# Kernel optimization log

Measured on AMD Instinct MI355X. Metric: run time of the kernel, lower is better.

The kernel has to match this reference:

```python
import jax, jax.numpy as jnp
import numpy as np

# TTCReward hyperparameters (init_kwargs)
LONG_TH = 0.0
LAT_TH = 0.0
H = 4               # num_historical_intervals
LEAST_MIN_TTC = 0.95
DT = 0.5            # time_span_per_interval

NUM_EGO = 32        # scenes (len(ptr) - 1)
AGENTS_PER = 128
N_AGENTS = NUM_EGO * AGENTS_PER   # 4096
T_TOTAL = 34


def setup_inputs():
    key = jax.random.key(0)
    k1, k2, k3, k4 = jax.random.split(key, 4)
    infer_position = jax.random.uniform(k1, (N_AGENTS, T_TOTAL, 2), jnp.float32) * 100.0
    infer_heading = (jax.random.uniform(k2, (N_AGENTS, T_TOTAL), jnp.float32) - 0.5) * (2.0 * np.pi)
    box = jax.random.uniform(k3, (N_AGENTS, 4), jnp.float32) * 1.5 + 0.5  # front/rear/left/right extents
    infer_valid_mask = jax.random.uniform(k4, (N_AGENTS, T_TOTAL)) > 0.05
    batch = jnp.repeat(jnp.arange(NUM_EGO, dtype=jnp.int32), AGENTS_PER)
    ptr = jnp.arange(NUM_EGO + 1, dtype=jnp.int32) * AGENTS_PER
    return dict(infer_position=infer_position, infer_heading=infer_heading, box=box,
                infer_valid_mask=infer_valid_mask, batch=batch, ptr=ptr)


def _corners(pos, yaw, box):
    # pos [N,T,2], yaw [N,T], box [N,4] = (front, rear, left, right) extents
    f, r, l, rt = box[:, 0], box[:, 1], box[:, 2], box[:, 3]
    local = jnp.stack([jnp.stack([f, l], -1), jnp.stack([f, -rt], -1),
                       jnp.stack([-r, -rt], -1), jnp.stack([-r, l], -1)], axis=1)  # [N,4,2]
    c = jnp.cos(yaw)[:, :, None]
    s = jnp.sin(yaw)[:, :, None]
    lx = local[:, None, :, 0]
    ly = local[:, None, :, 1]
    x = lx * c - ly * s + pos[:, :, None, 0]
    y = lx * s + ly * c + pos[:, :, None, 1]
    return jnp.stack([x, y], -1)  # [N,T,4,2]


def _loss(lx, ly, bf, br, bl, brt):
    # min over 4 box-side clamped penetrations, then max over the 4 corners (last axis)
    long_t = jnp.minimum(jnp.maximum(bf + LONG_TH - lx, 0.0),
                         jnp.maximum(br + LONG_TH + lx, 0.0))
    lat_t = jnp.minimum(jnp.maximum(bl + LAT_TH - ly, 0.0),
                        jnp.maximum(brt + LAT_TH + ly, 0.0))
    return jnp.max(jnp.minimum(long_t, lat_t), axis=-1)


def reference(infer_position, infer_heading, box, infer_valid_mask, batch, ptr):
    N = infer_heading.shape[0]
    vel = (infer_position[:, H:] - infer_position[:, H - 1:-1]) / DT
    pos = infer_position[:, H:] + vel * LEAST_MIN_TTC           # [N,T,2] position at min-TTC horizon
    yaw = infer_heading[:, H:]                                  # [N,T]
    corner = _corners(pos, yaw, box)                            # [N,T,4,2]

    ego = ptr[:-1]                                              # [B]
    B = ego.shape[0]
    Tn = pos.shape[1]

    ego_pos = jnp.swapaxes(pos[ego], 0, 1)                      # [T,B,2]
    ego_yaw = jnp.swapaxes(yaw[ego], 0, 1)                      # [T,B]
    ego_corner = jnp.swapaxes(corner[ego], 0, 1)                # [T,B,4,2]
    ego_box = box[ego]                                          # [B,4]
    agent_pos = jnp.swapaxes(pos, 0, 1)                         # [T,N,2]
    agent_yaw = jnp.swapaxes(yaw, 0, 1)                         # [T,N]
    agent_corner = jnp.swapaxes(corner, 0, 1)                   # [T,N,4,2]

    valid = infer_valid_mask[:, H:]                             # [N,T]
    edge_mask = (valid[ego].T[:, :, None] & valid.T[:, None, :]
                 & (batch[ego][:, None] == batch[None, :])[None]
                 & (ego[:, None] != jnp.arange(N)[None, :])[None])  # [T,B,N]

    # ego corners expressed in each agent's local frame, vs agent box
    d = ego_corner[:, :, None] - agent_pos[:, None, :, None]   # [T,B,N,4,2]
    ca = jnp.cos(agent_yaw)[:, None, :, None]
    sa = jnp.sin(agent_yaw)[:, None, :, None]
    ego_in_agent = _loss(d[..., 0] * ca + d[..., 1] * sa,
                         -d[..., 0] * sa + d[..., 1] * ca,
                         box[:, 0][None, None, :, None], box[:, 1][None, None, :, None],
                         box[:, 2][None, None, :, None], box[:, 3][None, None, :, None])  # [T,B,N]

    # agent corners expressed in each ego's local frame, vs ego box
    d2 = agent_corner[:, None] - ego_pos[:, :, None, None]     # [T,B,N,4,2]
    ce = jnp.cos(ego_yaw)[:, :, None, None]
    se = jnp.sin(ego_yaw)[:, :, None, None]
    agent_in_ego = _loss(d2[..., 0] * ce + d2[..., 1] * se,
                         -d2[..., 0] * se + d2[..., 1] * ce,
                         ego_box[:, 0][None, :, None, None], ego_box[:, 1][None, :, None, None],
                         ego_box[:, 2][None, :, None, None], ego_box[:, 3][None, :, None, None])  # [T,B,N]

    # Replicate original dense_to_sparse edge orderings: ego_in_agent edges enumerate
    # edge_mask in (t,i,j) order; agent_in_ego edges use the transposed (t,j,i) order.
    # The torch code max-combines the two lists per *position* e before scatter_max
    # over rows t*B+i (taken from the (t,i,j) ordering), which we reproduce exactly
    # via rank-based scatters into fixed-size [E] buffers.
    E = Tn * B * N
    rows = jnp.broadcast_to((jnp.arange(Tn)[:, None] * B + jnp.arange(B)[None, :])[:, :, None],
                            (Tn, B, N)).reshape(-1)
    m = edge_mask.reshape(-1)
    idx = jnp.where(m, jnp.cumsum(m.astype(jnp.int32)) - 1, E)      # OOB index E -> dropped
    mT = jnp.swapaxes(edge_mask, 1, 2).reshape(-1)
    idxT = jnp.where(mT, jnp.cumsum(mT.astype(jnp.int32)) - 1, E)
    neg_inf = jnp.float32(-jnp.inf)
    b_by_rank = jnp.full((E,), neg_inf).at[idx].set(ego_in_agent.reshape(-1))
    a_by_rank = jnp.full((E,), neg_inf).at[idxT].set(jnp.swapaxes(agent_in_ego, 1, 2).reshape(-1))
    rows_by_rank = jnp.zeros((E,), jnp.int32).at[idx].set(rows.astype(jnp.int32))
    ttc_loss = jnp.maximum(a_by_rank, b_by_rank)
    seg_max = jax.ops.segment_max(ttc_loss, rows_by_rank, num_segments=Tn * B)  # empty -> -inf
    # reward per ego: all timesteps have max ttc_loss <= 0 (no edge -> -inf -> True)
    return jnp.all((seg_max <= 0.0).reshape(Tn, B), axis=0).astype(jnp.float32)
```

## Files before the change

kernel.cpp:

```cpp
#include <hip/hip_runtime.h>
#include <math.h>

#define NUM_EGO    32
#define AGENTS_PER 128
#define T_TOTAL    34
#define H_OFF      4
#define TN         30
#define SCALE      1.9f

__global__ __launch_bounds__(AGENTS_PER) void ttc_main(
    const float* __restrict__ posg,
    const float* __restrict__ headg,
    const float* __restrict__ boxg,
    const int*   __restrict__ validg,
    const int*   __restrict__ ptrg,
    float* __restrict__ out)
{
    const int blk = blockIdx.x;
    const int b   = blk / TN;
    const int t   = blk % TN;
    const int tt  = t + H_OFF;
    const int a   = threadIdx.x;

    const int e0 = ptrg[b];
    const int n  = e0 + a;

    const int   ev   = validg[e0 * T_TOTAL + tt];
    const float2 ep1 = *(const float2*)&posg[(e0 * T_TOTAL + tt) * 2];
    const float2 ep0 = *(const float2*)&posg[(e0 * T_TOTAL + tt - 1) * 2];
    const float eyaw = headg[e0 * T_TOTAL + tt];
    const float4 ebx = *(const float4*)&boxg[e0 * 4];
    const int   av   = validg[n * T_TOTAL + tt];
    const float2 ap1 = *(const float2*)&posg[(n * T_TOTAL + tt) * 2];
    const float2 ap0 = *(const float2*)&posg[(n * T_TOTAL + tt - 1) * 2];
    const float ayaw = headg[n * T_TOTAL + tt];
    const float4 abx = *(const float4*)&boxg[n * 4];

    const float ex = ep1.x + SCALE * (ep1.x - ep0.x);
    const float ey = ep1.y + SCALE * (ep1.y - ep0.y);
    const float ax = ap1.x + SCALE * (ap1.x - ap0.x);
    const float ay = ap1.y + SCALE * (ap1.y - ap0.y);
    const float ce = __cosf(eyaw), se = __sinf(eyaw);
    const float ca = __cosf(ayaw), sa = __sinf(ayaw);

    const float ef = ebx.x, er = ebx.y, el = ebx.z, ert = ebx.w;
    const float af = abx.x, ar = abx.y, al = abx.z, art = abx.w;

    const float elx[4] = { ef,  ef, -er, -er };
    const float ely[4] = { el, -ert, -ert,  el };
    const float alx[4] = { af,  af, -ar, -ar };
    const float aly[4] = { al, -art, -art,  al };

    float L1 = 0.0f;
    #pragma unroll
    for (int k = 0; k < 4; ++k) {
        float cxw = elx[k] * ce - ely[k] * se + ex;
        float cyw = elx[k] * se + ely[k] * ce + ey;
        float dx = cxw - ax;
        float dy = cyw - ay;
        float lx =  dx * ca + dy * sa;
        float ly = -dx * sa + dy * ca;
        float lo = fminf(fmaxf(af - lx, 0.0f), fmaxf(ar + lx, 0.0f));
        float la = fminf(fmaxf(al - ly, 0.0f), fmaxf(art + ly, 0.0f));
        L1 = fmaxf(L1, fminf(lo, la));
    }

    float L2 = 0.0f;
    #pragma unroll
    for (int k = 0; k < 4; ++k) {
        float cxw = alx[k] * ca - aly[k] * sa + ax;
        float cyw = alx[k] * sa + aly[k] * ca + ay;
        float dx = cxw - ex;
        float dy = cyw - ey;
        float lx =  dx * ce + dy * se;
        float ly = -dx * se + dy * ce;
        float lo = fminf(fmaxf(ef - lx, 0.0f), fmaxf(er + lx, 0.0f));
        float la = fminf(fmaxf(el - ly, 0.0f), fmaxf(ert + ly, 0.0f));
        L2 = fmaxf(L2, fminf(lo, la));
    }

    const bool hit = (a != 0) & (ev != 0) & (av != 0) &
                     (fmaxf(L1, L2) > 0.0f);

    if (__any(hit) && (threadIdx.x & 63) == 0) {
        out[b] = 0.0f;
    }
}

extern "C" void kernel_launch(void* const* d_in, const int* in_sizes, int n_in,
                              void* d_out, int out_size, void* d_ws, size_t ws_size,
                              hipStream_t stream) {
    const float* posg   = (const float*)d_in[0];
    const float* headg  = (const float*)d_in[1];
    const float* boxg   = (const float*)d_in[2];
    const int*   validg = (const int*)  d_in[3];
    const int*   ptrg   = (const int*)  d_in[5];
    float* out = (float*)d_out;

    hipMemsetD32Async((hipDeviceptr_t)out, 0x3F800000, NUM_EGO, stream);
    ttc_main<<<NUM_EGO * TN, AGENTS_PER, 0, stream>>>(
        posg, headg, boxg, validg, ptrg, out);
}
```

Measured before the change: 67.51 us.

## Fuse timesteps into one block per ego and drop separate memset

Launches one 768-thread block per ego scene, with six groups of threads each walking five consecutive timesteps. Previous positions are carried forward between steps, and sincos is computed in one call. A shared-memory OR reduction now writes the final 0/1 output directly, so the memset launch is no longer needed. This removes one launch and the cross-block writes, but only 32 blocks run, which leaves most of the GPU idle and lengthens each thread's serial work.

```diff
diff --git a/kernel.cpp b/kernel.cpp
--- a/kernel.cpp
+++ b/kernel.cpp
@@ -8,7 +8,11 @@
 #define TN         30
 #define SCALE      1.9f
 
-__global__ __launch_bounds__(AGENTS_PER) void ttc_main(
+#define BLOCK  768
+#define TPG    5
+#define NWAVES (BLOCK / 64)
+
+__global__ __launch_bounds__(BLOCK) void ttc_fused(
     const float* __restrict__ posg,
     const float* __restrict__ headg,
     const float* __restrict__ boxg,
@@ -16,33 +20,15 @@
     const int*   __restrict__ ptrg,
     float* __restrict__ out)
 {
-    const int blk = blockIdx.x;
-    const int b   = blk / TN;
-    const int t   = blk % TN;
-    const int tt  = t + H_OFF;
-    const int a   = threadIdx.x;
+    const int b   = blockIdx.x;
+    const int tid = threadIdx.x;
+    const int a   = tid & (AGENTS_PER - 1);
+    const int g   = tid >> 7;
+    const int e0  = ptrg[b];
+    const int n   = e0 + a;
 
-    const int e0 = ptrg[b];
-    const int n  = e0 + a;
-
-    const int   ev   = validg[e0 * T_TOTAL + tt];
-    const float2 ep1 = *(const float2*)&posg[(e0 * T_TOTAL + tt) * 2];
-    const float2 ep0 = *(const float2*)&posg[(e0 * T_TOTAL + tt - 1) * 2];
-    const float eyaw = headg[e0 * T_TOTAL + tt];
     const float4 ebx = *(const float4*)&boxg[e0 * 4];
-    const int   av   = validg[n * T_TOTAL + tt];
-    const float2 ap1 = *(const float2*)&posg[(n * T_TOTAL + tt) * 2];
-    const float2 ap0 = *(const float2*)&posg[(n * T_TOTAL + tt - 1) * 2];
-    const float ayaw = headg[n * T_TOTAL + tt];
     const float4 abx = *(const float4*)&boxg[n * 4];
-
-    const float ex = ep1.x + SCALE * (ep1.x - ep0.x);
-    const float ey = ep1.y + SCALE * (ep1.y - ep0.y);
-    const float ax = ap1.x + SCALE * (ap1.x - ap0.x);
-    const float ay = ap1.y + SCALE * (ap1.y - ap0.y);
-    const float ce = __cosf(eyaw), se = __sinf(eyaw);
-    const float ca = __cosf(ayaw), sa = __sinf(ayaw);
-
     const float ef = ebx.x, er = ebx.y, el = ebx.z, ert = ebx.w;
     const float af = abx.x, ar = abx.y, al = abx.z, art = abx.w;
 
@@ -51,39 +37,76 @@
     const float alx[4] = { af,  af, -ar, -ar };
     const float aly[4] = { al, -art, -art,  al };
 
-    float L1 = 0.0f;
+    bool anyhit = false;
+
+    const int t0  = g * TPG;
+    const int tt0 = t0 + H_OFF;
+    float2 eprev = *(const float2*)&posg[(e0 * T_TOTAL + tt0 - 1) * 2];
+    float2 aprev = *(const float2*)&posg[(n  * T_TOTAL + tt0 - 1) * 2];
+
     #pragma unroll
-    for (int k = 0; k < 4; ++k) {
-        float cxw = elx[k] * ce - ely[k] * se + ex;
-        float cyw = elx[k] * se + ely[k] * ce + ey;
-        float dx = cxw - ax;
-        float dy = cyw - ay;
-        float lx =  dx * ca + dy * sa;
-        float ly = -dx * sa + dy * ca;
-        float lo = fminf(fmaxf(af - lx, 0.0f), fmaxf(ar + lx, 0.0f));
-        float la = fminf(fmaxf(al - ly, 0.0f), fmaxf(art + ly, 0.0f));
-        L1 = fmaxf(L1, fminf(lo, la));
+    for (int i = 0; i < TPG; ++i) {
+        const int tt = tt0 + i;
+
+        const int    ev   = validg[e0 * T_TOTAL + tt];
+        const int    av   = validg[n  * T_TOTAL + tt];
+        const float2 ecur = *(const float2*)&posg[(e0 * T_TOTAL + tt) * 2];
+        const float2 acur = *(const float2*)&posg[(n  * T_TOTAL + tt) * 2];
+        const float  eyaw = headg[e0 * T_TOTAL + tt];
+        const float  ayaw = headg[n  * T_TOTAL + tt];
+
+        const float ex = ecur.x + SCALE * (ecur.x - eprev.x);
+        const float ey = ecur.y + SCALE * (ecur.y - eprev.y);
+        const float ax = acur.x + SCALE * (acur.x - aprev.x);
+        const float ay = acur.y + SCALE * (acur.y - aprev.y);
+        eprev = ecur; aprev = acur;
+
+        float se, ce, sa, ca;
+        __sincosf(eyaw, &se, &ce);
+        __sincosf(ayaw, &sa, &ca);
+
+        float L1 = 0.0f;
+        #pragma unroll
+        for (int k = 0; k < 4; ++k) {
+            float cxw = elx[k] * ce - ely[k] * se + ex;
+            float cyw = elx[k] * se + ely[k] * ce + ey;
+            float dx = cxw - ax;
+            float dy = cyw - ay;
+            float lx =  dx * ca + dy * sa;
+            float ly = -dx * sa + dy * ca;
+            float lo = fminf(fmaxf(af - lx, 0.0f), fmaxf(ar + lx, 0.0f));
+            float la = fminf(fmaxf(al - ly, 0.0f), fmaxf(art + ly, 0.0f));
+            L1 = fmaxf(L1, fminf(lo, la));
+        }
+
+        float L2 = 0.0f;
+        #pragma unroll
+        for (int k = 0; k < 4; ++k) {
+            float cxw = alx[k] * ca - aly[k] * sa + ax;
+            float cyw = alx[k] * sa + aly[k] * ca + ay;
+            float dx = cxw - ex;
+            float dy = cyw - ey;
+            float lx =  dx * ce + dy * se;
+            float ly = -dx * se + dy * ce;
+            float lo = fminf(fmaxf(ef - lx, 0.0f), fmaxf(er + lx, 0.0f));
+            float la = fminf(fmaxf(el - ly, 0.0f), fmaxf(ert + ly, 0.0f));
+            L2 = fmaxf(L2, fminf(lo, la));
+        }
+
+        anyhit |= (a != 0) & (ev != 0) & (av != 0) &
+                  (fmaxf(L1, L2) > 0.0f);
     }
 
-    float L2 = 0.0f;
-    #pragma unroll
-    for (int k = 0; k < 4; ++k) {
-        float cxw = alx[k] * ca - aly[k] * sa + ax;
-        float cyw = alx[k] * sa + aly[k] * ca + ay;
-        float dx = cxw - ex;
-        float dy = cyw - ey;
-        float lx =  dx * ce + dy * se;
-        float ly = -dx * se + dy * ce;
-        float lo = fminf(fmaxf(ef - lx, 0.0f), fmaxf(er + lx, 0.0f));
-        float la = fminf(fmaxf(el - ly, 0.0f), fmaxf(ert + ly, 0.0f));
-        L2 = fmaxf(L2, fminf(lo, la));
-    }
-
-    const bool hit = (a != 0) & (ev != 0) & (av != 0) &
-                     (fmaxf(L1, L2) > 0.0f);
-
-    if (__any(hit) && (threadIdx.x & 63) == 0) {
-        out[b] = 0.0f;
+    __shared__ int wflag[NWAVES];
+    const int w = tid >> 6;
+    const int hitw = __any(anyhit) ? 1 : 0;
+    if ((tid & 63) == 0) wflag[w] = hitw;
+    __syncthreads();
+    if (tid == 0) {
+        int f = 0;
+        #pragma unroll
+        for (int i = 0; i < NWAVES; ++i) f |= wflag[i];
+        out[b] = f ? 0.0f : 1.0f;
     }
 }
 
@@ -97,7 +120,6 @@
     const int*   ptrg   = (const int*)  d_in[5];
     float* out = (float*)d_out;
 
-    hipMemsetD32Async((hipDeviceptr_t)out, 0x3F800000, NUM_EGO, stream);
-    ttc_main<<<NUM_EGO * TN, AGENTS_PER, 0, stream>>>(
+    ttc_fused<<<NUM_EGO, BLOCK, 0, stream>>>(
         posg, headg, boxg, validg, ptrg, out);
 }
```

Result: slower. 69.28 us (+2.6%).
